# Optimization experiments

Measured on AMD Instinct MI355X. Metric: run time of the kernel, lower is better.

The kernel has to match this reference:

```python
import jax, jax.numpy as jnp
import numpy as np


def setup_inputs() -> dict:
    key = jax.random.key(0)
    k1, k2, k3, k4 = jax.random.split(key, 4)
    B, C_in, C_out, S = 128, 32, 8, 8192
    return {
        "x": jax.random.normal(k1, (B, C_in, S), dtype=jnp.float32),
        "w1": jax.random.normal(k2, (C_in, C_in, S), dtype=jnp.float32),
        "w2": jax.random.normal(k3, (C_out, C_in, S), dtype=jnp.float32),
        "bias": jax.random.normal(k4, (C_out, S), dtype=jnp.float32),
    }


def reference(x, w1, w2, bias):
    # Stage 1: (x.unsqueeze(1) * w1).sum(1) in torch sums the BROADCAST dim i,
    # so it reduces to an elementwise scale: out[b,j,s] = x[b,j,s] * sum_i w1[i,j,s]
    h = jnp.tanh(x * jnp.sum(w1, axis=0))            # (B, C_in, S)
    # Stage 2: true per-position contraction over the in-channel axis j
    out = jnp.einsum('bjs,ojs->bos', h, w2) + bias   # (B, C_out, S)
    return jnp.tanh(out)
```

## Files before the change

kernel.cpp:

```cpp
#include <hip/hip_runtime.h>
#include <cstddef>

#define SLEN 8192
#define CIN  32
#define COUT 8
#define BATCH 128
#define BCHUNK 4

typedef float v2f __attribute__((ext_vector_type(2)));
typedef float v4f __attribute__((ext_vector_type(4)));

__device__ __forceinline__ float fast_tanh(float x) {
    float t = __expf(2.0f * x);
    return 1.0f - 2.0f * __builtin_amdgcn_rcpf(t + 1.0f);
}

__global__ __launch_bounds__(256) void lc3_wsum(const float* __restrict__ w1,
                                                float* __restrict__ wsum) {
    __shared__ v4f part[4][64];
    const int tx = threadIdx.x & 63;
    const int ty = threadIdx.x >> 6;
    const int g  = blockIdx.x * 64 + tx;
    const int j  = g >> 11;
    const int s4 = g & 2047;

    v4f acc = (v4f)(0.f);
    #pragma unroll
    for (int ii = 0; ii < 8; ++ii) {
        const int i = ty * 8 + ii;
        acc += *reinterpret_cast<const v4f*>(
            &w1[(size_t)(i * CIN + j) * SLEN + (size_t)s4 * 4]);
    }
    part[ty][tx] = acc;
    __syncthreads();
    if (ty == 0) {
        v4f r = part[0][tx] + part[1][tx] + part[2][tx] + part[3][tx];
        *reinterpret_cast<v4f*>(&wsum[(size_t)j * SLEN + (size_t)s4 * 4]) = r;
    }
}

__global__ __launch_bounds__(256) void lc3_main(const float* __restrict__ x,
                                                const float* __restrict__ w2,
                                                const float* __restrict__ bias,
                                                const float* __restrict__ wsum,
                                                float* __restrict__ out) {
    const int s  = (blockIdx.x * 256 + threadIdx.x) * 2;
    const int b0 = blockIdx.y * BCHUNK;

    v2f acc[BCHUNK][COUT];
    #pragma unroll
    for (int k = 0; k < BCHUNK; ++k)
        #pragma unroll
        for (int o = 0; o < COUT; ++o) acc[k][o] = (v2f)(0.f);

    for (int j = 0; j < CIN; ++j) {
        const v2f wsv = *reinterpret_cast<const v2f*>(&wsum[j * SLEN + s]);
        v2f h[BCHUNK];
        #pragma unroll
        for (int k = 0; k < BCHUNK; ++k) {
            const v2f xv = *reinterpret_cast<const v2f*>(&x[((b0 + k) * CIN + j) * SLEN + s]);
            h[k].x = fast_tanh(xv.x * wsv.x);
            h[k].y = fast_tanh(xv.y * wsv.y);
        }
        #pragma unroll
        for (int o = 0; o < COUT; ++o) {
            const v2f wv = *reinterpret_cast<const v2f*>(&w2[(o * CIN + j) * SLEN + s]);
            #pragma unroll
            for (int k = 0; k < BCHUNK; ++k) {
                acc[k][o].x = fmaf(h[k].x, wv.x, acc[k][o].x);
                acc[k][o].y = fmaf(h[k].y, wv.y, acc[k][o].y);
            }
        }
    }

    #pragma unroll
    for (int o = 0; o < COUT; ++o) {
        const v2f bv = *reinterpret_cast<const v2f*>(&bias[o * SLEN + s]);
        #pragma unroll
        for (int k = 0; k < BCHUNK; ++k) {
            v2f r;
            r.x = fast_tanh(acc[k][o].x + bv.x);
            r.y = fast_tanh(acc[k][o].y + bv.y);
            *reinterpret_cast<v2f*>(&out[((b0 + k) * COUT + o) * SLEN + s]) = r;
        }
    }
}

extern "C" void kernel_launch(void* const* d_in, const int* in_sizes, int n_in,
                              void* d_out, int out_size, void* d_ws, size_t ws_size,
                              hipStream_t stream) {
    const float* x    = (const float*)d_in[0];
    const float* w1   = (const float*)d_in[1];
    const float* w2   = (const float*)d_in[2];
    const float* bias = (const float*)d_in[3];
    float* out  = (float*)d_out;
    float* wsum = (float*)d_ws;

    lc3_wsum<<<dim3(CIN * SLEN / 4 / 64), dim3(256), 0, stream>>>(w1, wsum);

    dim3 grid(SLEN / 2 / 256, BATCH / BCHUNK);
    lc3_main<<<grid, dim3(256), 0, stream>>>(x, w2, bias, wsum, out);
}
```

Baseline: 47.08 us.

## Transpose w2 per position, split channel reduction across half-blocks, prescale exp2

Adds a pre-pass that transposes w2 so each position's 8 output weights per input channel sit contiguously, letting the main kernel load them as wide vectors. The main kernel splits the 32-channel reduction between two halves of each block and combines them through shared memory, which doubles the number of threads working per output. The tanh arguments are prescaled by 2*log2(e) so a raw v_exp_f32 can be used. In exchange it adds an extra kernel launch, extra workspace traffic, and per-thread strided transposed-weight loads that may coalesce poorly.

```diff
diff --git a/kernel.cpp b/kernel.cpp
--- a/kernel.cpp
+++ b/kernel.cpp
@@ -5,13 +5,17 @@
 #define CIN  32
 #define COUT 8
 #define BATCH 128
-#define BCHUNK 4
+#define BK 4
+#define LOG2E2 2.885390081777927f
 
 typedef float v2f __attribute__((ext_vector_type(2)));
 typedef float v4f __attribute__((ext_vector_type(4)));
 
-__device__ __forceinline__ float fast_tanh(float x) {
-    float t = __expf(2.0f * x);
+__device__ __forceinline__ float exp2_fast(float x) {
+    float r; asm("v_exp_f32 %0, %1" : "=v"(r) : "v"(x)); return r;
+}
+__device__ __forceinline__ float tanh_scaled(float v) {
+    float t = exp2_fast(v);
     return 1.0f - 2.0f * __builtin_amdgcn_rcpf(t + 1.0f);
 }
 
@@ -34,54 +38,104 @@
     part[ty][tx] = acc;
     __syncthreads();
     if (ty == 0) {
-        v4f r = part[0][tx] + part[1][tx] + part[2][tx] + part[3][tx];
+        v4f r = (part[0][tx] + part[1][tx] + part[2][tx] + part[3][tx]) * LOG2E2;
         *reinterpret_cast<v4f*>(&wsum[(size_t)j * SLEN + (size_t)s4 * 4]) = r;
     }
 }
 
-__global__ __launch_bounds__(256) void lc3_main(const float* __restrict__ x,
-                                                const float* __restrict__ w2,
-                                                const float* __restrict__ bias,
-                                                const float* __restrict__ wsum,
-                                                float* __restrict__ out) {
-    const int s  = (blockIdx.x * 256 + threadIdx.x) * 2;
-    const int b0 = blockIdx.y * BCHUNK;
+__global__ __launch_bounds__(256) void lc3_w2t(const float* __restrict__ w2,
+                                               float* __restrict__ w2t) {
+    const int lane = threadIdx.x & 63;
+    const int wv   = threadIdx.x >> 6;
+    const int sp   = blockIdx.x * 64 + lane;
+    const int jp   = blockIdx.y * 4 + wv;
+    #pragma unroll
+    for (int jj = 0; jj < 2; ++jj) {
+        const int j = jp * 2 + jj;
+        v2f a[COUT];
+        #pragma unroll
+        for (int o = 0; o < COUT; ++o)
+            a[o] = *reinterpret_cast<const v2f*>(&w2[(size_t)(o * CIN + j) * SLEN + sp * 2]);
+        float* dst = &w2t[((size_t)sp * CIN + j) * COUT * 2];
+        #pragma unroll
+        for (int c = 0; c < 4; ++c) {
+            v4f q = { a[2*c].x, a[2*c].y, a[2*c+1].x, a[2*c+1].y };
+            *reinterpret_cast<v4f*>(&dst[c * 4]) = q;
+        }
+    }
+}
 
-    v2f acc[BCHUNK][COUT];
+__global__ __launch_bounds__(256, 4) void lc3_main(const float* __restrict__ x,
+                                                   const float* __restrict__ w2t,
+                                                   const float* __restrict__ bias,
+                                                   const float* __restrict__ wsum,
+                                                   float* __restrict__ out) {
+    __shared__ v2f part[BK * COUT][128];
+    const int tl = threadIdx.x & 127;
+    const int jh = threadIdx.x >> 7;
+    const int sp = blockIdx.x * 128 + tl;
+    const int s  = sp * 2;
+    const int b0 = blockIdx.y * BK;
+    const int jb = jh * 16;
+
+    v2f acc[BK][COUT];
     #pragma unroll
-    for (int k = 0; k < BCHUNK; ++k)
+    for (int k = 0; k < BK; ++k)
         #pragma unroll
         for (int o = 0; o < COUT; ++o) acc[k][o] = (v2f)(0.f);
 
-    for (int j = 0; j < CIN; ++j) {
-        const v2f wsv = *reinterpret_cast<const v2f*>(&wsum[j * SLEN + s]);
-        v2f h[BCHUNK];
+    const float* wp  = wsum + (size_t)jb * SLEN + s;
+    const float* w2p = w2t + ((size_t)sp * CIN + jb) * COUT * 2;
+    const float* xk[BK];
+    #pragma unroll
+    for (int k = 0; k < BK; ++k)
+        xk[k] = x + ((size_t)(b0 + k) * CIN + jb) * SLEN + s;
+
+    #pragma unroll 2
+    for (int j = 0; j < 16; ++j) {
+        const v2f wsv = *reinterpret_cast<const v2f*>(&wp[(size_t)j * SLEN]);
+        const v4f w01 = *reinterpret_cast<const v4f*>(&w2p[j * 16 + 0]);
+        const v4f w23 = *reinterpret_cast<const v4f*>(&w2p[j * 16 + 4]);
+        const v4f w45 = *reinterpret_cast<const v4f*>(&w2p[j * 16 + 8]);
+        const v4f w67 = *reinterpret_cast<const v4f*>(&w2p[j * 16 + 12]);
         #pragma unroll
-        for (int k = 0; k < BCHUNK; ++k) {
-            const v2f xv = *reinterpret_cast<const v2f*>(&x[((b0 + k) * CIN + j) * SLEN + s]);
-            h[k].x = fast_tanh(xv.x * wsv.x);
-            h[k].y = fast_tanh(xv.y * wsv.y);
-        }
-        #pragma unroll
-        for (int o = 0; o < COUT; ++o) {
-            const v2f wv = *reinterpret_cast<const v2f*>(&w2[(o * CIN + j) * SLEN + s]);
-            #pragma unroll
-            for (int k = 0; k < BCHUNK; ++k) {
-                acc[k][o].x = fmaf(h[k].x, wv.x, acc[k][o].x);
-                acc[k][o].y = fmaf(h[k].y, wv.y, acc[k][o].y);
-            }
+        for (int k = 0; k < BK; ++k) {
+            const v2f xv = *reinterpret_cast<const v2f*>(&xk[k][(size_t)j * SLEN]);
+            const v2f v = xv * wsv;
+            v2f h;
+            h.x = tanh_scaled(v.x);
+            h.y = tanh_scaled(v.y);
+            acc[k][0] += h * w01.xy;
+            acc[k][1] += h * w01.zw;
+            acc[k][2] += h * w23.xy;
+            acc[k][3] += h * w23.zw;
+            acc[k][4] += h * w45.xy;
+            acc[k][5] += h * w45.zw;
+            acc[k][6] += h * w67.xy;
+            acc[k][7] += h * w67.zw;
         }
     }
 
-    #pragma unroll
-    for (int o = 0; o < COUT; ++o) {
-        const v2f bv = *reinterpret_cast<const v2f*>(&bias[o * SLEN + s]);
+    if (jh) {
         #pragma unroll
-        for (int k = 0; k < BCHUNK; ++k) {
-            v2f r;
-            r.x = fast_tanh(acc[k][o].x + bv.x);
-            r.y = fast_tanh(acc[k][o].y + bv.y);
-            *reinterpret_cast<v2f*>(&out[((b0 + k) * COUT + o) * SLEN + s]) = r;
+        for (int k = 0; k < BK; ++k)
+            #pragma unroll
+            for (int o = 0; o < COUT; ++o)
+                part[k * COUT + o][tl] = acc[k][o];
+    }
+    __syncthreads();
+    if (!jh) {
+        #pragma unroll
+        for (int o = 0; o < COUT; ++o) {
+            const v2f bv = *reinterpret_cast<const v2f*>(&bias[o * SLEN + s]);
+            #pragma unroll
+            for (int k = 0; k < BK; ++k) {
+                const v2f t = (acc[k][o] + part[k * COUT + o][tl] + bv) * LOG2E2;
+                v2f r;
+                r.x = tanh_scaled(t.x);
+                r.y = tanh_scaled(t.y);
+                *reinterpret_cast<v2f*>(&out[((size_t)(b0 + k) * COUT + o) * SLEN + s]) = r;
+            }
         }
     }
 }
@@ -95,9 +149,10 @@
     const float* bias = (const float*)d_in[3];
     float* out  = (float*)d_out;
     float* wsum = (float*)d_ws;
+    float* w2t  = (float*)((char*)d_ws + (size_t)CIN * SLEN * 4);
 
     lc3_wsum<<<dim3(CIN * SLEN / 4 / 64), dim3(256), 0, stream>>>(w1, wsum);
-
-    dim3 grid(SLEN / 2 / 256, BATCH / BCHUNK);
-    lc3_main<<<grid, dim3(256), 0, stream>>>(x, w2, bias, wsum, out);
+    lc3_w2t<<<dim3(64, 4), dim3(256), 0, stream>>>(w2, w2t);
+    dim3 grid(SLEN / 256, BATCH / BK);
+    lc3_main<<<grid, dim3(256), 0, stream>>>(x, w2t, bias, wsum, out);
 }
```

New measurement: 79.25 us. 1.68x slower.
